# Performance work log

Hardware: AMD Instinct MI355X
Metric: run time of the kernel (lower is better)

Reference implementation:

```python
import jax, jax.numpy as jnp
import numpy as np

EMBED_DIM = 1024
NUM_HEADS = 16
HEAD_DIM = EMBED_DIM // NUM_HEADS
B, N = 4, 2048


def setup_inputs() -> dict:
    key = jax.random.key(0)
    ks = jax.random.split(key, 12)
    s = 1.0 / np.sqrt(EMBED_DIM)
    inp = {
        "x": jax.random.normal(ks[0], (B, N, EMBED_DIM), dtype=jnp.float32),
        "dist_matrix": jax.random.uniform(ks[1], (N, N), dtype=jnp.float32),
        # Linear weights stored torch-style [out, in]
        "Wq": jax.random.normal(ks[2], (EMBED_DIM, EMBED_DIM), dtype=jnp.float32) * s,
        "bq": jnp.zeros((EMBED_DIM,), dtype=jnp.float32),
        "Wk": jax.random.normal(ks[3], (EMBED_DIM, EMBED_DIM), dtype=jnp.float32) * s,
        "bk": jnp.zeros((EMBED_DIM,), dtype=jnp.float32),
        "Wv": jax.random.normal(ks[4], (EMBED_DIM, EMBED_DIM), dtype=jnp.float32) * s,
        "bv": jnp.zeros((EMBED_DIM,), dtype=jnp.float32),
        "Wo": jax.random.normal(ks[5], (EMBED_DIM, EMBED_DIM), dtype=jnp.float32) * s,
        "bo": jnp.zeros((EMBED_DIM,), dtype=jnp.float32),
        # DistanceBias params: bias = dist_w * dist + dist_b (learned scalar affine)
        "dist_w": jnp.asarray(-1.0, dtype=jnp.float32),
        "dist_b": jnp.asarray(0.0, dtype=jnp.float32),
    }
    return inp


def reference(x, dist_matrix, Wq, bq, Wk, bk, Wv, bv, Wo, bo, dist_w, dist_b):
    b, n, c = x.shape
    h, d = NUM_HEADS, HEAD_DIM
    # projections (torch Linear: x @ W.T + b), reshape to [b, h, n, d]
    def proj(W, bias):
        y = jnp.einsum('bnc,oc->bno', x, W) + bias
        return y.reshape(b, n, h, d).transpose(0, 2, 1, 3)
    q = proj(Wq, bq)
    k = proj(Wk, bk)
    v = proj(Wv, bv)
    scores = jnp.einsum('bhnd,bhmd->bhnm', q, k) / np.sqrt(d).astype(np.float32)
    bias = dist_w * dist_matrix + dist_b            # [N, N], shared over b, h
    scores = scores + bias[None, None, :, :]
    attn = jax.nn.softmax(scores, axis=-1)
    out = jnp.einsum('bhnm,bhmd->bhnd', attn, v)    # [b, h, n, d]
    out = out.transpose(0, 2, 1, 3).reshape(b, n, c)
    return jnp.einsum('bnc,oc->bno', out, Wo) + bo
```

## Files before the change

### kernel.cpp

```cpp
#include <hip/hip_runtime.h>
#include <stdint.h>

typedef unsigned short ushort;
typedef __attribute__((ext_vector_type(8))) short bf16x8;
typedef __attribute__((ext_vector_type(4))) float f32x4;
typedef __attribute__((ext_vector_type(16))) float f32x16;

__device__ __forceinline__ float b2f(ushort u) {
    return __uint_as_float(((unsigned)u) << 16);
}
__device__ __forceinline__ ushort f2b(float f) {
    unsigned u = __float_as_uint(f);
    u += 0x7fff + ((u >> 16) & 1);
    return (ushort)(u >> 16);
}

#if __has_builtin(__builtin_amdgcn_exp2f)
#define EXP2(x) __builtin_amdgcn_exp2f(x)
#else
#define EXP2(x) __expf((x) * 0.69314718056f)
#endif

__device__ __forceinline__ unsigned cvtpk(float a, float b) {
    unsigned r;
    asm("v_cvt_pk_bf16_f32 %0, %1, %2" : "=v"(r) : "v"(a), "v"(b));
    return r;
}

__device__ __forceinline__ void plswap(unsigned &a, unsigned &b) {
#if __has_builtin(__builtin_amdgcn_permlane32_swap)
    auto r = __builtin_amdgcn_permlane32_swap(a, b, 0, 0);
    a = (unsigned)r[0]; b = (unsigned)r[1];
#else
    asm volatile("v_permlane32_swap_b32 %0, %1" : "+v"(a), "+v"(b));
#endif
}

#define SEQN 2048
#define EMB  1024
#define NH   16
#define HD   64
#define BHSTRIDE (SEQN * HD)

__device__ __forceinline__ void gload16(const ushort* g, ushort* l) {
    __builtin_amdgcn_global_load_lds(
        (const __attribute__((address_space(1))) unsigned int*)g,
        (__attribute__((address_space(3))) unsigned int*)l, 16, 0, 0);
}

__global__ __launch_bounds__(256) void conv_x(
        const float* __restrict__ s, ushort* __restrict__ d) {
    const size_t i = (size_t)blockIdx.x * 256 + threadIdx.x;
    float4 a = ((const float4*)s)[2 * i];
    float4 b = ((const float4*)s)[2 * i + 1];
    ushort pk[8] = {f2b(a.x), f2b(a.y), f2b(a.z), f2b(a.w),
                    f2b(b.x), f2b(b.y), f2b(b.z), f2b(b.w)};
    ((uint4*)d)[i] = *(uint4*)pk;
}

__global__ __launch_bounds__(256) void conv_w4(
        const float* __restrict__ W0, const float* __restrict__ W1,
        const float* __restrict__ W2, const float* __restrict__ W3,
        ushort* __restrict__ d) {
    const float* s = (blockIdx.y == 0) ? W0 : (blockIdx.y == 1) ? W1
                   : (blockIdx.y == 2) ? W2 : W3;
    ushort* dst = d + ((size_t)blockIdx.y << 20);
    const size_t i = (size_t)blockIdx.x * 256 + threadIdx.x;
    float4 a = ((const float4*)s)[2 * i];
    float4 b = ((const float4*)s)[2 * i + 1];
    ushort pk[8] = {f2b(a.x), f2b(a.y), f2b(a.z), f2b(a.w),
                    f2b(b.x), f2b(b.y), f2b(b.z), f2b(b.w)};
    ((uint4*)dst)[i] = *(uint4*)pk;
}

__global__ __launch_bounds__(256) void conv_Lp(
        const float* __restrict__ dist, const float* __restrict__ dw,
        const float* __restrict__ db, float* __restrict__ Lp) {
    const float c1 = dw[0] * 1.44269504f, c2 = db[0] * 1.44269504f;
    const size_t gid = (size_t)blockIdx.x * 256 + threadIdx.x;
    const int lo  = (int)(gid & 31);
    const int kv4 = (int)((gid >> 5) & 511);
    const int qt  = (int)(gid >> 14);
    const int q   = qt * 32 + lo;
    float4 d = *(const float4*)(dist + (size_t)q * SEQN + kv4 * 4);
    float4 o = {fmaf(d.x, c1, c2), fmaf(d.y, c1, c2),
                fmaf(d.z, c1, c2), fmaf(d.w, c1, c2)};
    ((float4*)Lp)[gid] = o;
}

#define LDSZ (128 * 32)

__global__ __launch_bounds__(256) void gemm_qkv(
        const ushort* __restrict__ xb, const ushort* __restrict__ Wb,
        const float* __restrict__ bq, const float* __restrict__ bk,
        const float* __restrict__ bv,
        ushort* __restrict__ qb, ushort* __restrict__ kb,
        ushort* __restrict__ vT) {
    __shared__ ushort As[2][LDSZ];
    __shared__ ushort Bs[2][LDSZ];
    const int m0   = blockIdx.x * 128;
    const int nt   = blockIdx.y;
    const int wsel = nt >> 3;
    const int n0   = (nt & 7) * 128;
    const ushort* W    = Wb + ((size_t)wsel << 20);
    const float* bias  = (wsel == 0) ? bq : (wsel == 1) ? bk : bv;

    const int t = threadIdx.x, lane = t & 63, wave = t >> 6;
    const int ln = lane & 15, quad = lane >> 4;
    const int wm = wave & 1, wn = wave >> 1;

    const int e0 = wave * 128 + lane;
    const int e1 = e0 + 64;
    const ushort* gA0 = xb + (size_t)(m0 + (e0 >> 2)) * 1024 + (e0 & 3) * 8;
    const ushort* gA1 = xb + (size_t)(m0 + (e1 >> 2)) * 1024 + (e1 & 3) * 8;
    const ushort* gB0 = W  + (size_t)(n0 + (e0 >> 2)) * 1024 + (e0 & 3) * 8;
    const ushort* gB1 = W  + (size_t)(n0 + (e1 >> 2)) * 1024 + (e1 & 3) * 8;
    ushort* lA0a = &As[0][wave * 1024]; ushort* lA0b = lA0a + 512;
    ushort* lA1a = &As[1][wave * 1024]; ushort* lA1b = lA1a + 512;
    ushort* lB0a = &Bs[0][wave * 1024]; ushort* lB0b = lB0a + 512;
    ushort* lB1a = &Bs[1][wave * 1024]; ushort* lB1b = lB1a + 512;

    f32x4 acc[4][4];
#pragma unroll
    for (int i = 0; i < 4; i++)
#pragma unroll
        for (int j = 0; j < 4; j++) acc[i][j] = (f32x4){0.f, 0.f, 0.f, 0.f};

    for (int k0 = 0; k0 < 1024; k0 += 64) {
        __syncthreads();
        gload16(gA0 + k0,      lA0a); gload16(gA1 + k0,      lA0b);
        gload16(gB0 + k0,      lB0a); gload16(gB1 + k0,      lB0b);
        gload16(gA0 + k0 + 32, lA1a); gload16(gA1 + k0 + 32, lA1b);
        gload16(gB0 + k0 + 32, lB1a); gload16(gB1 + k0 + 32, lB1b);
        __syncthreads();
#pragma unroll
        for (int kk2 = 0; kk2 < 2; kk2++) {
            bf16x8 af[4], bfr[4];
#pragma unroll
            for (int i = 0; i < 4; i++)
                af[i]  = *(bf16x8*)&As[kk2][(wm * 64 + i * 16 + ln) * 32 + quad * 8];
#pragma unroll
            for (int j = 0; j < 4; j++)
                bfr[j] = *(bf16x8*)&Bs[kk2][(wn * 64 + j * 16 + ln) * 32 + quad * 8];
            if (wsel < 2) {
#pragma unroll
                for (int j = 0; j < 4; j++)
#pragma unroll
                    for (int i = 0; i < 4; i++)
                        acc[j][i] = __builtin_amdgcn_mfma_f32_16x16x32_bf16(
                                        bfr[j], af[i], acc[j][i], 0, 0, 0);
            } else {
#pragma unroll
                for (int i = 0; i < 4; i++)
#pragma unroll
                    for (int j = 0; j < 4; j++)
                        acc[i][j] = __builtin_amdgcn_mfma_f32_16x16x32_bf16(
                                        af[i], bfr[j], acc[i][j], 0, 0, 0);
            }
        }
    }

    if (wsel < 2) {
        ushort* dst = (wsel == 0) ? qb : kb;
        const float scale = (wsel == 0) ? 0.125f : 1.0f;
#pragma unroll
        for (int j = 0; j < 4; j++) {
            const int o0 = n0 + wn * 64 + j * 16 + quad * 4;
            const int h  = o0 >> 6, d0 = o0 & 63;
            const float b0 = bias[o0], b1 = bias[o0 + 1];
            const float b2 = bias[o0 + 2], b3 = bias[o0 + 3];
#pragma unroll
            for (int i = 0; i < 4; i++) {
                const int m  = m0 + wm * 64 + i * 16 + ln;
                const int bb = m >> 11;
                const int ns = m & 2047;
                uint2 pk2;
                pk2.x = cvtpk((acc[j][i][0] + b0) * scale,
                              (acc[j][i][1] + b1) * scale);
                pk2.y = cvtpk((acc[j][i][2] + b2) * scale,
                              (acc[j][i][3] + b3) * scale);
                *(uint2*)&dst[(size_t)(bb * NH + h) * BHSTRIDE +
                              (size_t)ns * HD + d0] = pk2;
            }
        }
    } else {
#pragma unroll
        for (int j = 0; j < 4; j++) {
            const int o  = n0 + wn * 64 + j * 16 + ln;
            const float bval = bias[o];
            const int h = o >> 6, d = o & 63;
#pragma unroll
            for (int i = 0; i < 4; i++) {
                const int mg = m0 + wm * 64 + i * 16 + quad * 4;
                const int b  = mg >> 11;
                const int ns = mg & 2047;
                uint2 pk2;
                pk2.x = cvtpk(acc[i][j][0] + bval, acc[i][j][1] + bval);
                pk2.y = cvtpk(acc[i][j][2] + bval, acc[i][j][3] + bval);
                *(uint2*)&vT[(size_t)(b * NH + h) * BHSTRIDE +
                             (size_t)d * SEQN + ns] = pk2;
            }
        }
    }
}

__global__ __launch_bounds__(256, 4) void attn(
        ushort* q,
        const ushort* __restrict__ k,
        const ushort* __restrict__ vT,
        const float* __restrict__ Lp) {
    __shared__ short Ks[2][64 * 72];
    __shared__ short Vs[2][64 * 72];
    const int t = threadIdx.x, lane = t & 63, wave = t >> 6;
    const int lo = lane & 31, hi = lane >> 5;
    const int wid  = blockIdx.x + (blockIdx.y << 4) + (blockIdx.z << 8);
    const int xcd  = wid & 7;
    const int slot = wid >> 3;
    const int bh   = xcd * 8 + (slot >> 4);
    const int qx   = slot & 15;
    const int qw0 = qx * 128 + wave * 32;

    ushort* qp = q + (size_t)bh * BHSTRIDE;
    const ushort* kp = k  + (size_t)bh * BHSTRIDE;
    const ushort* vp = vT + (size_t)bh * BHSTRIDE;
    const float4* Lp4 = (const float4*)Lp + ((size_t)(qw0 >> 5) * 512) * 32 + lo;

    const int sr = t >> 2;
    const int sc = (t & 3) * 16;

    bf16x8 qf[4];
#pragma unroll
    for (int kk = 0; kk < 4; kk++)
        qf[kk] = *(const bf16x8*)(qp + (size_t)(qw0 + lo) * HD + kk * 16 + hi * 8);

    f32x16 O[2];
#pragma unroll
    for (int dt = 0; dt < 2; dt++)
#pragma unroll
        for (int i = 0; i < 16; i++) O[dt][i] = 0.f;
    float lsum = 0.f;

    uint4 krg0 = *(const uint4*)(kp + (size_t)sr * HD + sc);
    uint4 krg1 = *(const uint4*)(kp + (size_t)sr * HD + sc + 8);
    uint4 vrg0 = *(const uint4*)(vp + (size_t)sr * SEQN + sc);
    uint4 vrg1 = *(const uint4*)(vp + (size_t)sr * SEQN + sc + 8);
    *(uint4*)&Ks[0][sr * 72 + sc]     = krg0;
    *(uint4*)&Ks[0][sr * 72 + sc + 8] = krg1;
    *(uint4*)&Vs[0][sr * 72 + sc]     = vrg0;
    *(uint4*)&Vs[0][sr * 72 + sc + 8] = vrg1;
    krg0 = *(const uint4*)(kp + (size_t)(64 + sr) * HD + sc);
    krg1 = *(const uint4*)(kp + (size_t)(64 + sr) * HD + sc + 8);
    vrg0 = *(const uint4*)(vp + (size_t)sr * SEQN + 64 + sc);
    vrg1 = *(const uint4*)(vp + (size_t)sr * SEQN + 64 + sc + 8);

    for (int kt = 0; kt < 32; kt++) {
        const int kv0 = kt * 64;
        const int cb = kt & 1;
        __syncthreads();
        *(uint4*)&Ks[cb ^ 1][sr * 72 + sc]     = krg0;
        *(uint4*)&Ks[cb ^ 1][sr * 72 + sc + 8] = krg1;
        *(uint4*)&Vs[cb ^ 1][sr * 72 + sc]     = vrg0;
        *(uint4*)&Vs[cb ^ 1][sr * 72 + sc + 8] = vrg1;
        const int kvn = (kv0 + 128) & 2047;
        krg0 = *(const uint4*)(kp + (size_t)(kvn + sr) * HD + sc);
        krg1 = *(const uint4*)(kp + (size_t)(kvn + sr) * HD + sc + 8);
        vrg0 = *(const uint4*)(vp + (size_t)sr * SEQN + kvn + sc);
        vrg1 = *(const uint4*)(vp + (size_t)sr * SEQN + kvn + sc + 8);
        float4 lv2[2][4];
#pragma unroll
        for (int s = 0; s < 2; s++)
#pragma unroll
            for (int n = 0; n < 4; n++)
                lv2[s][n] = Lp4[((kv0 >> 2) + s * 8 + hi + 2 * n) * 32];

#pragma unroll
        for (int s = 0; s < 2; s++) {
            f32x16 z;
#pragma unroll
            for (int i = 0; i < 16; i++) z[i] = 0.f;
            __builtin_amdgcn_s_setprio(1);
#pragma unroll
            for (int kk = 0; kk < 4; kk++) {
                bf16x8 kf = *(bf16x8*)&Ks[cb][(s * 32 + lo) * 72 + kk * 16 + hi * 8];
                z = __builtin_amdgcn_mfma_f32_32x32x16_bf16(kf, qf[kk], z, 0, 0, 0);
            }
            __builtin_amdgcn_s_setprio(0);
            float p[16];
#pragma unroll
            for (int n = 0; n < 4; n++) {
#pragma unroll
                for (int m = 0; m < 4; m++) {
                    float pv = EXP2(fmaf(z[n * 4 + m], 1.44269504f,
                                         ((const float*)&lv2[s][n])[m]));
                    lsum += pv;
                    p[n * 4 + m] = pv;
                }
            }
#pragma unroll
            for (int kl = 0; kl < 2; kl++) {
                unsigned a0 = cvtpk(p[kl * 8 + 0], p[kl * 8 + 1]);
                unsigned b0 = cvtpk(p[kl * 8 + 4], p[kl * 8 + 5]);
                plswap(a0, b0);
                unsigned a1 = cvtpk(p[kl * 8 + 2], p[kl * 8 + 3]);
                unsigned b1 = cvtpk(p[kl * 8 + 6], p[kl * 8 + 7]);
                plswap(a1, b1);
                union { bf16x8 v; unsigned u[4]; } pf;
                pf.u[0] = a0; pf.u[1] = a1; pf.u[2] = b0; pf.u[3] = b1;
                const int kvk = s * 2 + kl;
                __builtin_amdgcn_s_setprio(1);
#pragma unroll
                for (int dt = 0; dt < 2; dt++) {
                    bf16x8 vf = *(bf16x8*)&Vs[cb][(dt * 32 + lo) * 72 +
                                                  kvk * 16 + hi * 8];
                    O[dt] = __builtin_amdgcn_mfma_f32_32x32x16_bf16(
                                vf, pf.v, O[dt], 0, 0, 0);
                }
                __builtin_amdgcn_s_setprio(0);
            }
        }
    }

    float tot = lsum + __shfl_xor(lsum, 32);
    const float inv = 1.0f / tot;
#pragma unroll
    for (int dt = 0; dt < 2; dt++)
#pragma unroll
        for (int n = 0; n < 4; n++) {
            uint2 pk2;
            pk2.x = cvtpk(O[dt][n * 4 + 0] * inv, O[dt][n * 4 + 1] * inv);
            pk2.y = cvtpk(O[dt][n * 4 + 2] * inv, O[dt][n * 4 + 3] * inv);
            *(uint2*)(qp + (size_t)(qw0 + lo) * HD + dt * 32 + hi * 4 + n * 8)
                = pk2;
        }
}

__global__ __launch_bounds__(256) void gemm_out(
        const ushort* __restrict__ ao, const ushort* __restrict__ Wob,
        const float* __restrict__ bias, float* __restrict__ out) {
    __shared__ ushort As[2][LDSZ];
    __shared__ ushort Bs[2][LDSZ];
    const int m0 = blockIdx.x * 128;
    const int n0 = blockIdx.y * 128;
    const int t = threadIdx.x, lane = t & 63, wave = t >> 6;
    const int ln = lane & 15, quad = lane >> 4;
    const int wm = wave & 1, wn = wave >> 1;

    const int e0 = wave * 128 + lane;
    const int e1 = e0 + 64;
    const int bb = m0 >> 11;
    const int nbase = m0 & 2047;
    const ushort* gA0 = ao + ((size_t)bb << 21) +
                        (size_t)(nbase + (e0 >> 2)) * 64 + (e0 & 3) * 8;
    const ushort* gA1 = ao + ((size_t)bb << 21) +
                        (size_t)(nbase + (e1 >> 2)) * 64 + (e1 & 3) * 8;
    const ushort* gB0 = Wob + (size_t)(n0 + (e0 >> 2)) * 1024 + (e0 & 3) * 8;
    const ushort* gB1 = Wob + (size_t)(n0 + (e1 >> 2)) * 1024 + (e1 & 3) * 8;
    ushort* lA0a = &As[0][wave * 1024]; ushort* lA0b = lA0a + 512;
    ushort* lA1a = &As[1][wave * 1024]; ushort* lA1b = lA1a + 512;
    ushort* lB0a = &Bs[0][wave * 1024]; ushort* lB0b = lB0a + 512;
    ushort* lB1a = &Bs[1][wave * 1024]; ushort* lB1b = lB1a + 512;

    f32x4 acc[4][4];
#pragma unroll
    for (int i = 0; i < 4; i++)
#pragma unroll
        for (int j = 0; j < 4; j++) acc[i][j] = (f32x4){0.f, 0.f, 0.f, 0.f};

    for (int k0 = 0; k0 < 1024; k0 += 64) {
        const size_t aoff = ((size_t)(k0 >> 6) << 17);
        __syncthreads();
        gload16(gA0 + aoff,      lA0a); gload16(gA1 + aoff,      lA0b);
        gload16(gB0 + k0,        lB0a); gload16(gB1 + k0,        lB0b);
        gload16(gA0 + aoff + 32, lA1a); gload16(gA1 + aoff + 32, lA1b);
        gload16(gB0 + k0 + 32,   lB1a); gload16(gB1 + k0 + 32,   lB1b);
        __syncthreads();
#pragma unroll
        for (int kk2 = 0; kk2 < 2; kk2++) {
            bf16x8 af[4], bfr[4];
#pragma unroll
            for (int i = 0; i < 4; i++)
                af[i]  = *(bf16x8*)&As[kk2][(wm * 64 + i * 16 + ln) * 32 + quad * 8];
#pragma unroll
            for (int j = 0; j < 4; j++)
                bfr[j] = *(bf16x8*)&Bs[kk2][(wn * 64 + j * 16 + ln) * 32 + quad * 8];
#pragma unroll
            for (int i = 0; i < 4; i++)
#pragma unroll
                for (int j = 0; j < 4; j++)
                    acc[i][j] = __builtin_amdgcn_mfma_f32_16x16x32_bf16(
                                    af[i], bfr[j], acc[i][j], 0, 0, 0);
        }
    }

#pragma unroll
    for (int j = 0; j < 4; j++) {
        const int o = n0 + wn * 64 + j * 16 + ln;
        const float bval = bias[o];
#pragma unroll
        for (int i = 0; i < 4; i++) {
            const int mg = m0 + wm * 64 + i * 16 + quad * 4;
#pragma unroll
            for (int r = 0; r < 4; r++)
                out[(size_t)(mg + r) * EMB + o] = acc[i][j][r] + bval;
        }
    }
}

extern "C" void kernel_launch(void* const* d_in, const int* in_sizes, int n_in,
                              void* d_out, int out_size, void* d_ws, size_t ws_size,
                              hipStream_t stream) {
    const float* x    = (const float*)d_in[0];
    const float* dist = (const float*)d_in[1];
    const float* Wq   = (const float*)d_in[2];
    const float* bq   = (const float*)d_in[3];
    const float* Wk   = (const float*)d_in[4];
    const float* bk   = (const float*)d_in[5];
    const float* Wv   = (const float*)d_in[6];
    const float* bv   = (const float*)d_in[7];
    const float* Wo   = (const float*)d_in[8];
    const float* bo   = (const float*)d_in[9];
    const float* dw   = (const float*)d_in[10];
    const float* db   = (const float*)d_in[11];

    const size_t PLANE = (size_t)8192 * 1024;
    ushort* qb = (ushort*)d_ws;
    ushort* kb = qb + PLANE;
    ushort* xb = kb + PLANE;
    ushort* Wb = xb + PLANE;
    ushort* vT = (ushort*)d_out;
    float*  Lf = (float*)(vT + PLANE);

    dim3 blk(256);
    conv_x       <<<dim3(4096),      blk, 0, stream>>>(x, xb);
    conv_w4      <<<dim3(512, 4),    blk, 0, stream>>>(Wq, Wk, Wv, Wo, Wb);
    conv_Lp      <<<dim3(4096),      blk, 0, stream>>>(dist, dw, db, Lf);
    gemm_qkv     <<<dim3(64, 24),    blk, 0, stream>>>(xb, Wb, bq, bk, bv,
                                                       qb, kb, vT);
    attn         <<<dim3(16, 16, 4), blk, 0, stream>>>(qb, kb, vT, Lf);
    gemm_out     <<<dim3(64, 8),     blk, 0, stream>>>(qb, Wb + 3 * (size_t)(1 << 20),
                                                       bo, (float*)d_out);
}
```

Before: 319.2 us.

## Double-buffer LDS tiles in QKV and output projection GEMMs to overlap loads

```diff
diff --git a/kernel.cpp b/kernel.cpp
--- a/kernel.cpp
+++ b/kernel.cpp
@@ -115,10 +115,7 @@
     const ushort* gA1 = xb + (size_t)(m0 + (e1 >> 2)) * 1024 + (e1 & 3) * 8;
     const ushort* gB0 = W  + (size_t)(n0 + (e0 >> 2)) * 1024 + (e0 & 3) * 8;
     const ushort* gB1 = W  + (size_t)(n0 + (e1 >> 2)) * 1024 + (e1 & 3) * 8;
-    ushort* lA0a = &As[0][wave * 1024]; ushort* lA0b = lA0a + 512;
-    ushort* lA1a = &As[1][wave * 1024]; ushort* lA1b = lA1a + 512;
-    ushort* lB0a = &Bs[0][wave * 1024]; ushort* lB0b = lB0a + 512;
-    ushort* lB1a = &Bs[1][wave * 1024]; ushort* lB1b = lB1a + 512;
+    const int lofs = wave * 1024;
 
     f32x4 acc[4][4];
 #pragma unroll
@@ -126,38 +123,43 @@
 #pragma unroll
         for (int j = 0; j < 4; j++) acc[i][j] = (f32x4){0.f, 0.f, 0.f, 0.f};
 
-    for (int k0 = 0; k0 < 1024; k0 += 64) {
+    gload16(gA0, &As[0][lofs]); gload16(gA1, &As[0][lofs + 512]);
+    gload16(gB0, &Bs[0][lofs]); gload16(gB1, &Bs[0][lofs + 512]);
+    __syncthreads();
+
+#pragma unroll 2
+    for (int kt = 0; kt < 32; kt++) {
+        const int cur = kt & 1;
+        if (kt < 31) {
+            const int k0n = kt * 32 + 32;
+            gload16(gA0 + k0n, &As[cur ^ 1][lofs]);
+            gload16(gA1 + k0n, &As[cur ^ 1][lofs + 512]);
+            gload16(gB0 + k0n, &Bs[cur ^ 1][lofs]);
+            gload16(gB1 + k0n, &Bs[cur ^ 1][lofs + 512]);
+        }
+        bf16x8 af[4], bfr[4];
+#pragma unroll
+        for (int i = 0; i < 4; i++)
+            af[i]  = *(bf16x8*)&As[cur][(wm * 64 + i * 16 + ln) * 32 + quad * 8];
+#pragma unroll
+        for (int j = 0; j < 4; j++)
+            bfr[j] = *(bf16x8*)&Bs[cur][(wn * 64 + j * 16 + ln) * 32 + quad * 8];
+        if (wsel < 2) {
+#pragma unroll
+            for (int j = 0; j < 4; j++)
+#pragma unroll
+                for (int i = 0; i < 4; i++)
+                    acc[j][i] = __builtin_amdgcn_mfma_f32_16x16x32_bf16(
+                                    bfr[j], af[i], acc[j][i], 0, 0, 0);
+        } else {
+#pragma unroll
+            for (int i = 0; i < 4; i++)
+#pragma unroll
+                for (int j = 0; j < 4; j++)
+                    acc[i][j] = __builtin_amdgcn_mfma_f32_16x16x32_bf16(
+                                    af[i], bfr[j], acc[i][j], 0, 0, 0);
+        }
         __syncthreads();
-        gload16(gA0 + k0,      lA0a); gload16(gA1 + k0,      lA0b);
-        gload16(gB0 + k0,      lB0a); gload16(gB1 + k0,      lB0b);
-        gload16(gA0 + k0 + 32, lA1a); gload16(gA1 + k0 + 32, lA1b);
-        gload16(gB0 + k0 + 32, lB1a); gload16(gB1 + k0 + 32, lB1b);
-        __syncthreads();
-#pragma unroll
-        for (int kk2 = 0; kk2 < 2; kk2++) {
-            bf16x8 af[4], bfr[4];
-#pragma unroll
-            for (int i = 0; i < 4; i++)
-                af[i]  = *(bf16x8*)&As[kk2][(wm * 64 + i * 16 + ln) * 32 + quad * 8];
-#pragma unroll
-            for (int j = 0; j < 4; j++)
-                bfr[j] = *(bf16x8*)&Bs[kk2][(wn * 64 + j * 16 + ln) * 32 + quad * 8];
-            if (wsel < 2) {
-#pragma unroll
-                for (int j = 0; j < 4; j++)
-#pragma unroll
-                    for (int i = 0; i < 4; i++)
-                        acc[j][i] = __builtin_amdgcn_mfma_f32_16x16x32_bf16(
-                                        bfr[j], af[i], acc[j][i], 0, 0, 0);
-            } else {
-#pragma unroll
-                for (int i = 0; i < 4; i++)
-#pragma unroll
-                    for (int j = 0; j < 4; j++)
-                        acc[i][j] = __builtin_amdgcn_mfma_f32_16x16x32_bf16(
-                                        af[i], bfr[j], acc[i][j], 0, 0, 0);
-            }
-        }
     }
 
     if (wsel < 2) {
@@ -355,10 +357,7 @@
                         (size_t)(nbase + (e1 >> 2)) * 64 + (e1 & 3) * 8;
     const ushort* gB0 = Wob + (size_t)(n0 + (e0 >> 2)) * 1024 + (e0 & 3) * 8;
     const ushort* gB1 = Wob + (size_t)(n0 + (e1 >> 2)) * 1024 + (e1 & 3) * 8;
-    ushort* lA0a = &As[0][wave * 1024]; ushort* lA0b = lA0a + 512;
-    ushort* lA1a = &As[1][wave * 1024]; ushort* lA1b = lA1a + 512;
-    ushort* lB0a = &Bs[0][wave * 1024]; ushort* lB0b = lB0a + 512;
-    ushort* lB1a = &Bs[1][wave * 1024]; ushort* lB1b = lB1a + 512;
+    const int lofs = wave * 1024;
 
     f32x4 acc[4][4];
 #pragma unroll
@@ -366,30 +365,35 @@
 #pragma unroll
         for (int j = 0; j < 4; j++) acc[i][j] = (f32x4){0.f, 0.f, 0.f, 0.f};
 
-    for (int k0 = 0; k0 < 1024; k0 += 64) {
-        const size_t aoff = ((size_t)(k0 >> 6) << 17);
+    gload16(gA0, &As[0][lofs]); gload16(gA1, &As[0][lofs + 512]);
+    gload16(gB0, &Bs[0][lofs]); gload16(gB1, &Bs[0][lofs + 512]);
+    __syncthreads();
+
+#pragma unroll 2
+    for (int kt = 0; kt < 32; kt++) {
+        const int cur = kt & 1;
+        if (kt < 31) {
+            const int k0n = kt * 32 + 32;
+            const size_t aoffn = ((size_t)(k0n >> 6) << 17) + (k0n & 32);
+            gload16(gA0 + aoffn, &As[cur ^ 1][lofs]);
+            gload16(gA1 + aoffn, &As[cur ^ 1][lofs + 512]);
+            gload16(gB0 + k0n,   &Bs[cur ^ 1][lofs]);
+            gload16(gB1 + k0n,   &Bs[cur ^ 1][lofs + 512]);
+        }
+        bf16x8 af[4], bfr[4];
+#pragma unroll
+        for (int i = 0; i < 4; i++)
+            af[i]  = *(bf16x8*)&As[cur][(wm * 64 + i * 16 + ln) * 32 + quad * 8];
+#pragma unroll
+        for (int j = 0; j < 4; j++)
+            bfr[j] = *(bf16x8*)&Bs[cur][(wn * 64 + j * 16 + ln) * 32 + quad * 8];
+#pragma unroll
+        for (int i = 0; i < 4; i++)
+#pragma unroll
+            for (int j = 0; j < 4; j++)
+                acc[i][j] = __builtin_amdgcn_mfma_f32_16x16x32_bf16(
+                                af[i], bfr[j], acc[i][j], 0, 0, 0);
         __syncthreads();
-        gload16(gA0 + aoff,      lA0a); gload16(gA1 + aoff,      lA0b);
-        gload16(gB0 + k0,        lB0a); gload16(gB1 + k0,        lB0b);
-        gload16(gA0 + aoff + 32, lA1a); gload16(gA1 + aoff + 32, lA1b);
-        gload16(gB0 + k0 + 32,   lB1a); gload16(gB1 + k0 + 32,   lB1b);
-        __syncthreads();
-#pragma unroll
-        for (int kk2 = 0; kk2 < 2; kk2++) {
-            bf16x8 af[4], bfr[4];
-#pragma unroll
-            for (int i = 0; i < 4; i++)
-                af[i]  = *(bf16x8*)&As[kk2][(wm * 64 + i * 16 + ln) * 32 + quad * 8];
-#pragma unroll
-            for (int j = 0; j < 4; j++)
-                bfr[j] = *(bf16x8*)&Bs[kk2][(wn * 64 + j * 16 + ln) * 32 + quad * 8];
-#pragma unroll
-            for (int i = 0; i < 4; i++)
-#pragma unroll
-                for (int j = 0; j < 4; j++)
-                    acc[i][j] = __builtin_amdgcn_mfma_f32_16x16x32_bf16(
-                                    af[i], bfr[j], acc[i][j], 0, 0, 0);
-        }
     }
 
 #pragma unroll
```

Measured after the change: 325.4 us. About the same (+1.9%).
